# Kernel tuning notes

Measured on AMD Instinct MI355X. Metric: run time of the kernel, lower is better.

## Reference

```python
import jax, jax.numpy as jnp
import numpy as np
from jax import lax

B, T, K, HID, NCLS = 32, 2048, 17, 64, 10
DILATIONS = (1, 1, 2)
RESIDUAL = (False, True, True)
TK = 3  # temporal kernel
BN_EPS = 1e-5
LN_EPS = 1e-5

COCO_EDGES = [(0,1),(0,2),(1,3),(2,4),(5,6),(5,7),(7,9),(6,8),(8,10),(5,11),(6,12),(11,13),(13,15),(12,14),(14,16)]

def build_skeleton_adj(num_kpts=K):
    adj = np.eye(num_kpts, dtype=np.float32)
    for i, j in COCO_EDGES:
        adj[i, j] = 1.0
        adj[j, i] = 1.0
    adj = adj + np.eye(num_kpts, dtype=np.float32)
    deg = adj.sum(axis=1, keepdims=True)
    deg[deg == 0] = 1.0
    return adj / deg

def setup_inputs() -> dict:
    key = jax.random.key(0)
    ks = jax.random.split(key, 8)
    kpts = jax.random.normal(ks[0], (B, T, K, 3), dtype=jnp.float32)
    adj = jnp.asarray(build_skeleton_adj(K))
    gcn_w0 = jax.random.normal(ks[1], (3, HID), dtype=jnp.float32) * (1.0 / np.sqrt(3))
    gcn_w1 = jax.random.normal(ks[2], (HID, HID), dtype=jnp.float32) * (1.0 / np.sqrt(HID))
    gcn_w2 = jax.random.normal(ks[3], (HID, HID), dtype=jnp.float32) * (1.0 / np.sqrt(HID))
    tcn_w = jax.random.normal(ks[4], (3, HID, HID, TK, 1), dtype=jnp.float32) * (1.0 / np.sqrt(HID * TK))
    bn_scale = 1.0 + 0.1 * jax.random.normal(ks[5], (3, HID), dtype=jnp.float32)
    bn_bias = 0.1 * jax.random.normal(ks[6], (3, HID), dtype=jnp.float32)
    bn_mean = 0.1 * jax.random.normal(ks[7], (3, HID), dtype=jnp.float32)
    bn_var = 0.5 + jax.random.uniform(jax.random.fold_in(key, 7), (3, HID), dtype=jnp.float32)
    ln_scale = jnp.ones((HID,), dtype=jnp.float32)
    ln_bias = jnp.zeros((HID,), dtype=jnp.float32)
    fc_w = jax.random.normal(jax.random.fold_in(key, 8), (HID, NCLS), dtype=jnp.float32) * (1.0 / np.sqrt(HID))
    fc_b = jnp.zeros((NCLS,), dtype=jnp.float32)
    return dict(kpts=kpts, adj=adj, gcn_w0=gcn_w0, gcn_w1=gcn_w1, gcn_w2=gcn_w2,
                tcn_w=tcn_w, bn_scale=bn_scale, bn_bias=bn_bias, bn_mean=bn_mean,
                bn_var=bn_var, ln_scale=ln_scale, ln_bias=ln_bias, fc_w=fc_w, fc_b=fc_b)

def _stgn_block(x, adj, gw, tw, bs, bb, bm, bv, dilation, residual):
    # x: [B, C_in, T, K]
    y = jnp.einsum('bctk,kv->bctv', x, adj)          # graph conv over keypoints
    y = jnp.einsum('bitk,io->botk', y, gw)           # channel mixing (intended GCN weight)
    pad = (TK - 1) * dilation // 2
    y = lax.conv_general_dilated(y, tw, window_strides=(1, 1),
                                 padding=[(pad, pad), (0, 0)],
                                 rhs_dilation=(dilation, 1),
                                 dimension_numbers=('NCHW', 'OIHW', 'NCHW'))
    inv = (bs / jnp.sqrt(bv + BN_EPS))[None, :, None, None]
    y = y * inv + (bb - bs * bm / jnp.sqrt(bv + BN_EPS))[None, :, None, None]
    y = jax.nn.relu(y)
    if residual:
        y = y + x
    return y

def reference(kpts, adj, gcn_w0, gcn_w1, gcn_w2, tcn_w, bn_scale, bn_bias, bn_mean,
              bn_var, ln_scale, ln_bias, fc_w, fc_b):
    x = jnp.transpose(kpts, (0, 3, 1, 2))  # [B, 3, T, K]
    gws = (gcn_w0, gcn_w1, gcn_w2)
    for i in range(3):
        x = _stgn_block(x, adj, gws[i], tcn_w[i], bn_scale[i], bn_bias[i],
                        bn_mean[i], bn_var[i], DILATIONS[i], RESIDUAL[i])
    feat = x.mean(axis=(2, 3))  # [B, HID] temporal/spatial mean pool
    mu = feat.mean(axis=-1, keepdims=True)
    var = feat.var(axis=-1, keepdims=True)
    feat = (feat - mu) / jnp.sqrt(var + LN_EPS) * ln_scale + ln_bias
    return feat @ fc_w + fc_b  # [B, NCLS]
```

## Files before the change

kernel.cpp:

```cpp
#include <hip/hip_runtime.h>
#include <hip/hip_bf16.h>
#include <math.h>

#define T_DIM 2048
#define K_DIM 17
#define HID   64
#define B_DIM 32

typedef short s16x8 __attribute__((ext_vector_type(8)));
typedef unsigned u32x2 __attribute__((ext_vector_type(2)));
typedef float f32x4 __attribute__((ext_vector_type(4)));

__device__ __forceinline__ float bf2f(short u) {
    unsigned v = ((unsigned)(unsigned short)u) << 16;
    return __builtin_bit_cast(float, v);
}
__device__ __forceinline__ short f2bf(float f) {
    __hip_bfloat16 h = __float2bfloat16(f);
    return __builtin_bit_cast(short, h);
}
__device__ __forceinline__ short f2bf_fast(float f) {
    unsigned u = __builtin_bit_cast(unsigned, f);
    return (short)((u + 0x8000u) >> 16);
}
__device__ __forceinline__ unsigned pk2bf(float lo, float hi) {
    unsigned ul = __builtin_bit_cast(unsigned, lo);
    unsigned uh = __builtin_bit_cast(unsigned, hi);
    return ((ul + 0x8000u) >> 16) | ((uh + 0x8000u) & 0xFFFF0000u);
}

static constexpr int NBR_PTR[18] = {0,3,6,9,11,13,17,21,24,27,29,31,34,37,40,43,45,47};
static constexpr int NBR_K[47] = {
    0,1,2,  0,1,3,  0,2,4,  1,3,  2,4,
    5,6,7,11,  5,6,8,12,  5,7,9,  6,8,10,  7,9,  8,10,
    5,11,13,  6,12,14,  11,13,15,  12,14,16,  13,15,  14,16 };

__global__ void fold_weights_kernel(
    const float* __restrict__ gw0, const float* __restrict__ gw1,
    const float* __restrict__ gw2, const float* __restrict__ tcn,
    const float* __restrict__ bns, const float* __restrict__ bnb,
    const float* __restrict__ bnm, const float* __restrict__ bnv,
    short* __restrict__ effT0, short* __restrict__ effT12,
    float* __restrict__ bnc)
{
    int tid = blockIdx.x * blockDim.x + threadIdx.x;
    int stride = gridDim.x * blockDim.x;
    for (int idx = tid; idx < 2048; idx += stride) {
        int o = idx >> 5, k = idx & 31, dt = k >> 3, cin = k & 7;
        float s = 0.f;
        if (dt < 3 && cin < 3)
            for (int m = 0; m < 64; m++)
                s += gw0[cin * 64 + m] * tcn[(o * 64 + m) * 3 + dt];
        effT0[idx] = f2bf(s);
    }
    for (int idx = tid; idx < 24576; idx += stride) {
        int blk = idx / 12288;
        int r = idx - blk * 12288;
        int o = r / 192, k = r - o * 192, dt = k >> 6, c = k & 63;
        const float* gw = blk ? gw2 : gw1;
        const float* tw = tcn + (size_t)(blk + 1) * 64 * 64 * 3;
        float s = 0.f;
        for (int m = 0; m < 64; m++)
            s += gw[c * 64 + m] * tw[(o * 64 + m) * 3 + dt];
        effT12[idx] = f2bf(s);
    }
    for (int i = tid; i < 192; i += stride) {
        float inv = bns[i] * rsqrtf(bnv[i] + 1e-5f);
        bnc[i] = inv;
        bnc[192 + i] = bnb[i] - bnm[i] * inv;
    }
}

__global__ __launch_bounds__(256, 4) void stgcn_ab_kernel(
    const float* __restrict__ x, const float* __restrict__ adj,
    const short* __restrict__ effT0, const short* __restrict__ effT12,
    const float* __restrict__ bnc, short* __restrict__ y2)
{
    __shared__ float adj_s[289];
    __shared__ __align__(16) float xt[12 * 51];
    __shared__ __align__(16) short ybuf[170 * 72];

    const int tid = threadIdx.x;
    const int b = blockIdx.y;
    const int t0 = blockIdx.x * 8;
    const int lane = tid & 63, wave = tid >> 6;
    const int col = lane & 15, kgrp = lane >> 4;

    for (int i = tid; i < 289; i += 256) adj_s[i] = adj[i];
    {
        const int tbase = t0 - 2;
        const float* xb = x + (size_t)(b * T_DIM + tbase) * 51;
        for (int i = tid; i < 612; i += 256) {
            int tt = tbase + i / 51;
            xt[i] = (tt >= 0 && tt < T_DIM) ? xb[i] : 0.f;
        }
    }
    s16x8 af1 = *(const s16x8*)(effT0 + (wave * 16 + col) * 32 + kgrp * 8);
    s16x8 af2[6];
    #pragma unroll
    for (int kk = 0; kk < 6; kk++)
        af2[kk] = *(const s16x8*)(effT12 +
            (wave * 16 + col) * 192 + kk * 32 + kgrp * 8);
    __syncthreads();

    for (int tile = 0; tile < 11; tile++) {
        const int r = tile * 16 + col;
        const int me = r < 170 ? r : 169;
        const int s = (me * 241) >> 12;
        const int k = me - s * 17;
        s16x8 bfr = (s16x8){0,0,0,0,0,0,0,0};
        if (kgrp < 3) {
            const float* xp = &xt[(s + kgrp) * 51 + k * 3];
            bfr[0] = f2bf_fast(xp[0]);
            bfr[1] = f2bf_fast(xp[1]);
            bfr[2] = f2bf_fast(xp[2]);
        }
        f32x4 acc = __builtin_amdgcn_mfma_f32_16x16x32_bf16(
            af1, bfr, (f32x4){0.f, 0.f, 0.f, 0.f}, 0, 0, 0);
        if (r < 170) {
            u32x2 st;
            st[0] = pk2bf(acc[0], acc[1]);
            st[1] = pk2bf(acc[2], acc[3]);
            *(u32x2*)&ybuf[r * 72 + wave * 16 + kgrp * 4] = st;
        }
    }
    __syncthreads();

    for (int idx = tid; idx < 320; idx += 256) {
        const int tl = idx >> 5, oq = idx & 31, o0 = oq * 2;
        const int t = t0 - 1 + tl;
        const bool valid = (t >= 0) && (t < T_DIM);
        const float inv0 = bnc[o0], inv1 = bnc[o0 + 1];
        const float sh0 = bnc[192 + o0], sh1 = bnc[192 + o0 + 1];
        float zk0[17], zk1[17];
        #pragma unroll
        for (int k = 0; k < 17; k++) {
            unsigned u = *(const unsigned*)&ybuf[(tl * 17 + k) * 72 + o0];
            zk0[k] = bf2f((short)(u & 0xFFFF));
            zk1[k] = bf2f((short)(u >> 16));
        }
        #pragma unroll
        for (int v = 0; v < 17; v++) {
            float g0 = 0.f, g1 = 0.f;
            #pragma unroll
            for (int e = NBR_PTR[v]; e < NBR_PTR[v + 1]; e++) {
                int k = NBR_K[e];
                float w = adj_s[k * 17 + v];
                g0 += w * zk0[k]; g1 += w * zk1[k];
            }
            float v0 = valid ? fmaxf(g0 * inv0 + sh0, 0.f) : 0.f;
            float v1 = valid ? fmaxf(g1 * inv1 + sh1, 0.f) : 0.f;
            *(unsigned*)&ybuf[(tl * 17 + v) * 72 + o0] = pk2bf(v0, v1);
        }
    }
    __syncthreads();

    f32x4 acc2[9];
    #pragma unroll
    for (int t2 = 0; t2 < 9; t2++) acc2[t2] = (f32x4){0.f, 0.f, 0.f, 0.f};
    #pragma unroll
    for (int kk = 0; kk < 6; kk++) {
        #pragma unroll
        for (int t2 = 0; t2 < 9; t2++) {
            const int r = t2 * 16 + col;
            const int me = r < 136 ? r : 135;
            s16x8 bfr = *(const s16x8*)&ybuf[
                (me + 17 * (kk >> 1)) * 72 + (kk & 1) * 32 + kgrp * 8];
            acc2[t2] = __builtin_amdgcn_mfma_f32_16x16x32_bf16(
                af2[kk], bfr, acc2[t2], 0, 0, 0);
        }
    }
    unsigned rv[17];
    {
        const int tl = tid >> 5, o0 = (tid & 31) * 2;
        #pragma unroll
        for (int v = 0; v < 17; v++)
            rv[v] = *(const unsigned*)&ybuf[((tl + 1) * 17 + v) * 72 + o0];
    }
    __syncthreads();

    #pragma unroll
    for (int t2 = 0; t2 < 9; t2++) {
        const int r = t2 * 16 + col;
        if (r < 136) {
            u32x2 st;
            st[0] = pk2bf(acc2[t2][0], acc2[t2][1]);
            st[1] = pk2bf(acc2[t2][2], acc2[t2][3]);
            *(u32x2*)&ybuf[r * 72 + wave * 16 + kgrp * 4] = st;
        }
    }
    __syncthreads();

    {
        const int tl = tid >> 5, o0 = (tid & 31) * 2;
        const float inv0 = bnc[64 + o0], inv1 = bnc[64 + o0 + 1];
        const float sh0 = bnc[256 + o0], sh1 = bnc[256 + o0 + 1];
        float zk0[17], zk1[17];
        #pragma unroll
        for (int k = 0; k < 17; k++) {
            unsigned u = *(const unsigned*)&ybuf[(tl * 17 + k) * 72 + o0];
            zk0[k] = bf2f((short)(u & 0xFFFF));
            zk1[k] = bf2f((short)(u >> 16));
        }
        const size_t gout = ((size_t)(b * T_DIM + t0 + tl) * K_DIM) * 64;
        #pragma unroll
        for (int v = 0; v < 17; v++) {
            float g0 = 0.f, g1 = 0.f;
            #pragma unroll
            for (int e = NBR_PTR[v]; e < NBR_PTR[v + 1]; e++) {
                int k = NBR_K[e];
                float w = adj_s[k * 17 + v];
                g0 += w * zk0[k]; g1 += w * zk1[k];
            }
            float v0 = fmaxf(g0 * inv0 + sh0, 0.f) + bf2f((short)(rv[v] & 0xFFFF));
            float v1 = fmaxf(g1 * inv1 + sh1, 0.f) + bf2f((short)(rv[v] >> 16));
            *(unsigned*)&y2[gout + (size_t)v * 64 + o0] = pk2bf(v0, v1);
        }
    }
}

__global__ __launch_bounds__(256, 4) void stgcn_c_kernel(
    const short* __restrict__ y2, const float* __restrict__ adj,
    const short* __restrict__ effW3, const float* __restrict__ bnc,
    float* __restrict__ part, int b0)
{
    __shared__ float adj_s[289];
    __shared__ __align__(16) short ybuf[204 * 72];
    __shared__ float pr[8][64];

    const int tid = threadIdx.x;
    const int b = blockIdx.y;
    const int t0 = blockIdx.x * 8;
    const int lane = tid & 63, wave = tid >> 6;
    const int col = lane & 15, kgrp = lane >> 4;

    for (int i = tid; i < 289; i += 256) adj_s[i] = adj[i];
    s16x8 af3[6];
    #pragma unroll
    for (int kk = 0; kk < 6; kk++)
        af3[kk] = *(const s16x8*)(effW3 +
            (wave * 16 + col) * 192 + kk * 32 + kgrp * 8);

    {
        const int bLo = b * (T_DIM * 17);
        const int bHi = bLo + T_DIM * 17;
        const int g0r = bLo + (t0 - 2) * 17;
        for (int idx = tid; idx < 1632; idx += 256) {
            const int row = idx >> 3, c = idx & 7;
            const int gr = g0r + row;
            s16x8 v = (s16x8){0,0,0,0,0,0,0,0};
            if (gr >= bLo && gr < bHi)
                v = *(const s16x8*)(y2 + (size_t)gr * 64 + c * 8);
            *(s16x8*)&ybuf[row * 72 + c * 8] = v;
        }
    }
    __syncthreads();

    f32x4 acc3[9];
    #pragma unroll
    for (int t3 = 0; t3 < 9; t3++) acc3[t3] = (f32x4){0.f, 0.f, 0.f, 0.f};
    #pragma unroll
    for (int kk = 0; kk < 6; kk++) {
        #pragma unroll
        for (int t3 = 0; t3 < 9; t3++) {
            const int r = t3 * 16 + col;
            const int me = r < 136 ? r : 135;
            s16x8 bfr = *(const s16x8*)&ybuf[
                (me + 34 * (kk >> 1)) * 72 + (kk & 1) * 32 + kgrp * 8];
            acc3[t3] = __builtin_amdgcn_mfma_f32_16x16x32_bf16(
                af3[kk], bfr, acc3[t3], 0, 0, 0);
        }
    }
    float rs0 = 0.f, rs1 = 0.f;
    {
        const int tl = tid >> 5, o0 = (tid & 31) * 2;
        #pragma unroll
        for (int v = 0; v < 17; v++) {
            unsigned u = *(const unsigned*)&ybuf[((tl + 2) * 17 + v) * 72 + o0];
            rs0 += bf2f((short)(u & 0xFFFF));
            rs1 += bf2f((short)(u >> 16));
        }
    }
    __syncthreads();

    #pragma unroll
    for (int t3 = 0; t3 < 9; t3++) {
        const int r = t3 * 16 + col;
        if (r < 136) {
            u32x2 st;
            st[0] = pk2bf(acc3[t3][0], acc3[t3][1]);
            st[1] = pk2bf(acc3[t3][2], acc3[t3][3]);
            *(u32x2*)&ybuf[r * 72 + wave * 16 + kgrp * 4] = st;
        }
    }
    __syncthreads();

    {
        const int tl = tid >> 5, o0 = (tid & 31) * 2;
        const float inv0 = bnc[128 + o0], inv1 = bnc[128 + o0 + 1];
        const float sh0 = bnc[320 + o0], sh1 = bnc[320 + o0 + 1];
        float zk0[17], zk1[17];
        #pragma unroll
        for (int k = 0; k < 17; k++) {
            unsigned u = *(const unsigned*)&ybuf[(tl * 17 + k) * 72 + o0];
            zk0[k] = bf2f((short)(u & 0xFFFF));
            zk1[k] = bf2f((short)(u >> 16));
        }
        float ps0 = rs0, ps1 = rs1;
        #pragma unroll
        for (int v = 0; v < 17; v++) {
            float g0 = 0.f, g1 = 0.f;
            #pragma unroll
            for (int e = NBR_PTR[v]; e < NBR_PTR[v + 1]; e++) {
                int k = NBR_K[e];
                float w = adj_s[k * 17 + v];
                g0 += w * zk0[k]; g1 += w * zk1[k];
            }
            ps0 += fmaxf(g0 * inv0 + sh0, 0.f);
            ps1 += fmaxf(g1 * inv1 + sh1, 0.f);
        }
        *(float2*)&pr[tl][o0] = make_float2(ps0, ps1);
    }
    __syncthreads();
    if (tid < 64) {
        float s = 0.f;
        #pragma unroll
        for (int i = 0; i < 8; i++) s += pr[i][tid];
        part[((size_t)(b0 + b) * 256 + blockIdx.x) * 64 + tid] = s;
    }
}

__global__ __launch_bounds__(64) void finish_kernel(
    const float* __restrict__ part, const float* __restrict__ ln_s,
    const float* __restrict__ ln_b, const float* __restrict__ fc_w,
    const float* __restrict__ fc_b, float* __restrict__ out)
{
    const int b = blockIdx.x;
    const int c = threadIdx.x;
    float s = 0.f;
    for (int i = 0; i < 256; i++)
        s += part[((size_t)b * 256 + i) * 64 + c];
    float feat = s / (float)(T_DIM * K_DIM);

    float m = feat;
    #pragma unroll
    for (int off = 32; off > 0; off >>= 1) m += __shfl_down(m, off);
    m = __shfl(m, 0) / 64.f;
    float d = feat - m;
    float v = d * d;
    #pragma unroll
    for (int off = 32; off > 0; off >>= 1) v += __shfl_down(v, off);
    v = __shfl(v, 0) / 64.f;
    float norm = d * rsqrtf(v + 1e-5f) * ln_s[c] + ln_b[c];

    __shared__ float ns[64];
    ns[c] = norm;
    __syncthreads();
    if (c < 10) {
        float o = fc_b[c];
        for (int i = 0; i < 64; i++) o += ns[i] * fc_w[i * 10 + c];
        out[b * 10 + c] = o;
    }
}

extern "C" void kernel_launch(void* const* d_in, const int* in_sizes, int n_in,
                              void* d_out, int out_size, void* d_ws, size_t ws_size,
                              hipStream_t stream)
{
    const float* kpts = (const float*)d_in[0];
    const float* adj  = (const float*)d_in[1];
    const float* gw0  = (const float*)d_in[2];
    const float* gw1  = (const float*)d_in[3];
    const float* gw2  = (const float*)d_in[4];
    const float* tcn  = (const float*)d_in[5];
    const float* bns  = (const float*)d_in[6];
    const float* bnb  = (const float*)d_in[7];
    const float* bnm  = (const float*)d_in[8];
    const float* bnv  = (const float*)d_in[9];
    const float* lns  = (const float*)d_in[10];
    const float* lnb  = (const float*)d_in[11];
    const float* fcw  = (const float*)d_in[12];
    const float* fcb  = (const float*)d_in[13];
    float* out = (float*)d_out;

    float* bnc  = (float*)d_ws;
    float* part = bnc + 384;
    short* effT0  = (short*)(part + (size_t)B_DIM * 256 * 64);
    short* effT12 = effT0 + 2048;
    short* y2     = effT12 + 24576;
    const size_t fixed_bytes = 384 * 4 + (size_t)B_DIM * 256 * 64 * 4
                             + 2048 * 2 + 24576 * 2;
    const size_t y_per_b = (size_t)T_DIM * K_DIM * 64 * 2;

    int cb = B_DIM;
    while (cb > 1 && fixed_bytes + (size_t)cb * y_per_b > ws_size) cb >>= 1;

    fold_weights_kernel<<<64, 256, 0, stream>>>(gw0, gw1, gw2, tcn,
                                                bns, bnb, bnm, bnv,
                                                effT0, effT12, bnc);

    for (int b0 = 0; b0 < B_DIM; b0 += cb) {
        stgcn_ab_kernel<<<dim3(T_DIM / 8, cb), 256, 0, stream>>>(
            kpts + (size_t)b0 * T_DIM * K_DIM * 3, adj, effT0, effT12, bnc, y2);
        stgcn_c_kernel<<<dim3(T_DIM / 8, cb), 256, 0, stream>>>(
            y2, adj, effT12 + 12288, bnc, part, b0);
    }

    finish_kernel<<<B_DIM, 64, 0, stream>>>(part, lns, lnb, fcw, fcb, out);
}
```

Before: 256.9 us.

## Raise occupancy hints, alias reduction buffer into LDS, widen finish kernel

Raises the launch-bounds minimum blocks per CU from 4 to 5 on both main kernels, asking the compiler to cap register use so more waves can be resident. In the C kernel the per-block partial-sum array now reuses part of the already-consumed ybuf LDS region, which shrinks that kernel's LDS footprint. The finish kernel uses 256 threads that each reduce a quarter of the partial sums before combining them in shared memory, which shortens its serial loop. The tighter register cap may cause spills, and the aliasing depends on that ybuf region no longer being read when pr is written.

```diff
diff --git a/kernel.cpp b/kernel.cpp
--- a/kernel.cpp
+++ b/kernel.cpp
@@ -71,7 +71,7 @@
     }
 }
 
-__global__ __launch_bounds__(256, 4) void stgcn_ab_kernel(
+__global__ __launch_bounds__(256, 5) void stgcn_ab_kernel(
     const float* __restrict__ x, const float* __restrict__ adj,
     const short* __restrict__ effT0, const short* __restrict__ effT12,
     const float* __restrict__ bnc, short* __restrict__ y2)
@@ -219,14 +219,15 @@
     }
 }
 
-__global__ __launch_bounds__(256, 4) void stgcn_c_kernel(
+__global__ __launch_bounds__(256, 5) void stgcn_c_kernel(
     const short* __restrict__ y2, const float* __restrict__ adj,
     const short* __restrict__ effW3, const float* __restrict__ bnc,
     float* __restrict__ part, int b0)
 {
     __shared__ float adj_s[289];
     __shared__ __align__(16) short ybuf[204 * 72];
-    __shared__ float pr[8][64];
+
+    float* pr = (float*)&ybuf[136 * 72];
 
     const int tid = threadIdx.x;
     const int b = blockIdx.y;
@@ -319,47 +320,50 @@
             ps0 += fmaxf(g0 * inv0 + sh0, 0.f);
             ps1 += fmaxf(g1 * inv1 + sh1, 0.f);
         }
-        *(float2*)&pr[tl][o0] = make_float2(ps0, ps1);
+        *(float2*)&pr[tl * 64 + o0] = make_float2(ps0, ps1);
     }
     __syncthreads();
     if (tid < 64) {
         float s = 0.f;
         #pragma unroll
-        for (int i = 0; i < 8; i++) s += pr[i][tid];
+        for (int i = 0; i < 8; i++) s += pr[i * 64 + tid];
         part[((size_t)(b0 + b) * 256 + blockIdx.x) * 64 + tid] = s;
     }
 }
 
-__global__ __launch_bounds__(64) void finish_kernel(
+__global__ __launch_bounds__(256) void finish_kernel(
     const float* __restrict__ part, const float* __restrict__ ln_s,
     const float* __restrict__ ln_b, const float* __restrict__ fc_w,
     const float* __restrict__ fc_b, float* __restrict__ out)
 {
+    __shared__ float red[4][64];
+    __shared__ float ns[64];
     const int b = blockIdx.x;
-    const int c = threadIdx.x;
+    const int g = threadIdx.x >> 6, c = threadIdx.x & 63;
     float s = 0.f;
-    for (int i = 0; i < 256; i++)
-        s += part[((size_t)b * 256 + i) * 64 + c];
-    float feat = s / (float)(T_DIM * K_DIM);
-
-    float m = feat;
-    #pragma unroll
-    for (int off = 32; off > 0; off >>= 1) m += __shfl_down(m, off);
-    m = __shfl(m, 0) / 64.f;
-    float d = feat - m;
-    float v = d * d;
-    #pragma unroll
-    for (int off = 32; off > 0; off >>= 1) v += __shfl_down(v, off);
-    v = __shfl(v, 0) / 64.f;
-    float norm = d * rsqrtf(v + 1e-5f) * ln_s[c] + ln_b[c];
-
-    __shared__ float ns[64];
-    ns[c] = norm;
-    __syncthreads();
-    if (c < 10) {
-        float o = fc_b[c];
-        for (int i = 0; i < 64; i++) o += ns[i] * fc_w[i * 10 + c];
-        out[b * 10 + c] = o;
+    for (int j = 0; j < 64; j++)
+        s += part[((size_t)b * 256 + g * 64 + j) * 64 + c];
+    red[g][c] = s;
+    __syncthreads();
+    if (threadIdx.x < 64) {
+        float feat = (red[0][c] + red[1][c] + red[2][c] + red[3][c])
+                   / (float)(T_DIM * K_DIM);
+        float m = feat;
+        #pragma unroll
+        for (int off = 32; off > 0; off >>= 1) m += __shfl_down(m, off);
+        m = __shfl(m, 0) / 64.f;
+        float d = feat - m;
+        float v = d * d;
+        #pragma unroll
+        for (int off = 32; off > 0; off >>= 1) v += __shfl_down(v, off);
+        v = __shfl(v, 0) / 64.f;
+        ns[c] = d * rsqrtf(v + 1e-5f) * ln_s[c] + ln_b[c];
+    }
+    __syncthreads();
+    if (threadIdx.x < 10) {
+        float o = fc_b[threadIdx.x];
+        for (int i = 0; i < 64; i++) o += ns[i] * fc_w[i * 10 + threadIdx.x];
+        out[b * 10 + threadIdx.x] = o;
     }
 }
 
@@ -406,5 +410,5 @@
             y2, adj, effT12 + 12288, bnc, part, b0);
     }
 
-    finish_kernel<<<B_DIM, 64, 0, stream>>>(part, lns, lnb, fcw, fcb, out);
-}
+    finish_kernel<<<B_DIM, 256, 0, stream>>>(part, lns, lnb, fcw, fcb, out);
+}
```

Result: slower. 294.0 us (+14.4%).
